# Optimization experiments

Measured on AMD Instinct MI355X. Metric: run time of the kernel, lower is better.

Reference implementation:

```python
import jax, jax.numpy as jnp
import numpy as np

N = 50000
E = 800000


def gcn_conv(x, W, b, src, dst, n_nodes):
    # PyG GCNConv: add self-loops, symmetric deg^-1/2 normalization,
    # out[dst] += norm * (x @ W)[src], then bias.
    h = x @ W  # [N, out]
    src_sl = jnp.concatenate([src, jnp.arange(n_nodes, dtype=src.dtype)])
    dst_sl = jnp.concatenate([dst, jnp.arange(n_nodes, dtype=dst.dtype)])
    deg = jax.ops.segment_sum(jnp.ones_like(dst_sl, dtype=h.dtype), dst_sl,
                              num_segments=n_nodes)  # in-degree incl. self-loop
    dinv = jnp.where(deg > 0, jax.lax.rsqrt(deg), 0.0)
    norm = dinv[src_sl] * dinv[dst_sl]  # [E+N]
    msg = norm[:, None] * h[src_sl]  # gather + scale, [E+N, out]
    out = jax.ops.segment_sum(msg, dst_sl, num_segments=n_nodes)
    return out + b


def setup_inputs() -> dict:
    key = jax.random.key(0)
    ks = jax.random.split(key, 8)
    F, H, O = 128, 128, 64
    x = jax.random.normal(ks[0], (N, F), dtype=jnp.float32)
    edge_index = jax.random.randint(ks[1], (2, E), 0, N, dtype=jnp.int64)
    # Glorot-ish scaled weights
    W1 = jax.random.normal(ks[2], (F, H), dtype=jnp.float32) / np.sqrt(F)
    b1 = jnp.zeros((H,), dtype=jnp.float32)
    W2 = jax.random.normal(ks[3], (H, H), dtype=jnp.float32) / np.sqrt(H)
    b2 = jnp.zeros((H,), dtype=jnp.float32)
    W3 = jax.random.normal(ks[4], (H, O), dtype=jnp.float32) / np.sqrt(H)
    b3 = jnp.zeros((O,), dtype=jnp.float32)
    return {"x": x, "edge_index": edge_index, "W1": W1, "b1": b1,
            "W2": W2, "b2": b2, "W3": W3, "b3": b3}


def reference(x, edge_index, W1, b1, W2, b2, W3, b3):
    src, dst = edge_index[0], edge_index[1]
    h = gcn_conv(x, W1, b1, src, dst, N)
    h = jax.nn.elu(h)
    h = gcn_conv(h, W2, b2, src, dst, N)
    h = jax.nn.elu(h)
    h = gcn_conv(h, W3, b3, src, dst, N)
    return h
```

## Files before the change

kernel.cpp:

```cpp
#include <hip/hip_runtime.h>
#include <hip/hip_fp16.h>
#include <math.h>


#define NFEAT_IN 128
#define SCAN_CHUNK 2048
#define NSHARD 8

typedef _Float16 f16x8 __attribute__((ext_vector_type(8)));
typedef float f32x4 __attribute__((ext_vector_type(4)));

__global__ void zero_kernel(int4* __restrict__ p, int n4) {
    int i = blockIdx.x * blockDim.x + threadIdx.x;
    if (i < n4) { int4 z; z.x = z.y = z.z = z.w = 0; p[i] = z; }
}

__global__ __launch_bounds__(256) void count_kernel(const int* __restrict__ dst,
                                                    int* __restrict__ cnt,
                                                    int E, int shard_sz) {
    int shard = blockIdx.x & (NSHARD - 1);
    int blk = blockIdx.x >> 3;
    int nblk = gridDim.x >> 3;
    int lo = shard * shard_sz, hi = lo + shard_sz;
    int stride = nblk * blockDim.x;
    int E4 = E >> 2;
    for (int g = blk * blockDim.x + threadIdx.x; g < E4; g += stride) {
        int4 d = *(const int4*)&dst[g * 4];
        if (d.x >= lo && d.x < hi) atomicAdd(&cnt[d.x], 1);
        if (d.y >= lo && d.y < hi) atomicAdd(&cnt[d.y], 1);
        if (d.z >= lo && d.z < hi) atomicAdd(&cnt[d.z], 1);
        if (d.w >= lo && d.w < hi) atomicAdd(&cnt[d.w], 1);
    }
    if (blockIdx.x == 0 && threadIdx.x < (E & 3)) {
        int d = dst[(E & ~3) + threadIdx.x];
        atomicAdd(&cnt[d], 1);
    }
}

__global__ __launch_bounds__(256) void reduce_kernel(const int* __restrict__ cnt,
                                                     int* __restrict__ bsum, int n) {
    __shared__ int wtot[4];
    int b = blockIdx.x, t = threadIdx.x;
    int base = b * SCAN_CHUNK + t * 8;
    int s = 0;
    if (base + 8 <= n) {
        int4 a = *(const int4*)&cnt[base];
        int4 c = *(const int4*)&cnt[base + 4];
        s = a.x + a.y + a.z + a.w + c.x + c.y + c.z + c.w;
    } else {
        for (int i = 0; i < 8; ++i) if (base + i < n) s += cnt[base + i];
    }
    int lane = t & 63, wid = t >> 6;
    #pragma unroll
    for (int off = 32; off > 0; off >>= 1) s += __shfl_down(s, off, 64);
    if (lane == 0) wtot[wid] = s;
    __syncthreads();
    if (t == 0) bsum[b] = wtot[0] + wtot[1] + wtot[2] + wtot[3];
}

__global__ void scanb_kernel(int* __restrict__ bsum, int nb, int* __restrict__ offs,
                             int n, int2* __restrict__ esw, int E) {
    int lane = threadIdx.x;
    int v = (lane < nb) ? bsum[lane] : 0;
    int inc = v;
    #pragma unroll
    for (int off = 1; off < 64; off <<= 1) {
        int t = __shfl_up(inc, off, 64);
        if (lane >= off) inc += t;
    }
    if (lane < nb) bsum[lane] = inc - v;
    if (lane == 63) offs[n] = inc;
    if (lane < 16) { int2 z; z.x = 0; z.y = 0; esw[E + lane] = z; }
}

__global__ __launch_bounds__(256) void scan3_kernel(const int* __restrict__ cnt,
                                                    const int* __restrict__ bbase,
                                                    int* __restrict__ offs,
                                                    int* __restrict__ pos,
                                                    float* __restrict__ dinv, int n) {
    __shared__ int wtot[4];
    int b = blockIdx.x, t = threadIdx.x;
    int base = b * SCAN_CHUNK + t * 8;
    int v[8];
    #pragma unroll
    for (int i = 0; i < 8; ++i) v[i] = (base + i < n) ? cnt[base + i] : 0;
    int psum[8], s = 0;
    #pragma unroll
    for (int i = 0; i < 8; ++i) { psum[i] = s; s += v[i]; }
    int lane = t & 63, wid = t >> 6;
    int inc = s;
    #pragma unroll
    for (int off = 1; off < 64; off <<= 1) {
        int tt = __shfl_up(inc, off, 64);
        if (lane >= off) inc += tt;
    }
    if (lane == 63) wtot[wid] = inc;
    __syncthreads();
    int wb = 0;
    for (int w = 0; w < wid; ++w) wb += wtot[w];
    int tbase = bbase[b] + wb + (inc - s);
    #pragma unroll
    for (int i = 0; i < 8; ++i) {
        if (base + i < n) {
            int o = tbase + psum[i];
            offs[base + i] = o;
            pos[base + i] = o;
            dinv[base + i] = rsqrtf((float)(v[i] + 1));
        }
    }
}

__global__ __launch_bounds__(256) void fill_kernel(const int* __restrict__ src,
                                                   const int* __restrict__ dst,
                                                   int* __restrict__ pos,
                                                   const float* __restrict__ dinv,
                                                   int2* __restrict__ esw,
                                                   int E, int shard_sz) {
    int shard = blockIdx.x & (NSHARD - 1);
    int blk = blockIdx.x >> 3;
    int nblk = gridDim.x >> 3;
    int lo = shard * shard_sz;
    int hi = lo + shard_sz;
    int stride = nblk * blockDim.x;
    for (int i = blk * blockDim.x + threadIdx.x; i < E; i += stride) {
        int d = dst[i];
        if (d >= lo && d < hi) {
            int s = src[i];
            int p = atomicAdd(&pos[d], 1);
            int2 e;
            e.x = s;
            e.y = __float_as_int(dinv[s]);
            esw[p] = e;
        }
    }
}

__global__ __launch_bounds__(256) void convx_kernel(const float* __restrict__ x,
                                                    f16x8* __restrict__ Xf, int nchunk) {
    int i = blockIdx.x * blockDim.x + threadIdx.x;
    if (i >= nchunk) return;
    int m = i >> 4, kc = i & 15;
    float4 a = *(const float4*)&x[(size_t)m * 128 + kc * 8];
    float4 b = *(const float4*)&x[(size_t)m * 128 + kc * 8 + 4];
    f16x8 v;
    v[0] = (_Float16)a.x; v[1] = (_Float16)a.y; v[2] = (_Float16)a.z; v[3] = (_Float16)a.w;
    v[4] = (_Float16)b.x; v[5] = (_Float16)b.y; v[6] = (_Float16)b.z; v[7] = (_Float16)b.w;
    int kt = kc >> 2, sub = kc & 3;
    Xf[(size_t)((m >> 4) * 4 + kt) * 64 + sub * 16 + (m & 15)] = v;
}

template <int NT>
__global__ void wfrag_kernel(const float* __restrict__ W, f16x8* __restrict__ Wf) {
    constexpr int BN = NT * 16;
    int c = blockIdx.x * blockDim.x + threadIdx.x;
    if (c >= NT * 4 * 64) return;
    int nt = c >> 8;
    int kt = (c >> 6) & 3;
    int l = c & 63;
    int n = nt * 16 + (l & 15);
    int k0 = kt * 32 + (l >> 4) * 8;
    f16x8 v;
    #pragma unroll
    for (int j = 0; j < 8; ++j) v[j] = (_Float16)W[(size_t)(k0 + j) * BN + n];
    Wf[c] = v;
}

template <int NT>
__global__ __launch_bounds__(256) void mgemm_kernel(const f16x8* __restrict__ Xf,
                                                    const f16x8* __restrict__ Wg,
                                                    __half* __restrict__ Y, int mtiles) {
    constexpr int BN = NT * 16;
    __shared__ f16x8 Wf[NT * 4 * 64];
    int t = threadIdx.x;
    #pragma unroll
    for (int i = 0; i < NT; ++i) Wf[t + i * 256] = Wg[t + i * 256];
    __syncthreads();
    int lane = t & 63;
    int mtile = blockIdx.x * 4 + (t >> 6);
    if (mtile >= mtiles) return;
    const f16x8* xb = Xf + (size_t)mtile * 4 * 64;
    f16x8 bf[4];
    #pragma unroll
    for (int kt = 0; kt < 4; ++kt) bf[kt] = xb[kt * 64 + lane];
    f32x4 acc[NT];
    #pragma unroll
    for (int nt = 0; nt < NT; ++nt) acc[nt] = (f32x4){0.f, 0.f, 0.f, 0.f};
    #pragma unroll
    for (int kt = 0; kt < 4; ++kt) {
        #pragma unroll
        for (int nt = 0; nt < NT; ++nt) {
            f16x8 af = Wf[(nt * 4 + kt) * 64 + lane];
            acc[nt] = __builtin_amdgcn_mfma_f32_16x16x32_f16(af, bf[kt], acc[nt], 0, 0, 0);
        }
    }
    int m = mtile * 16 + (lane & 15);
    int nc0 = (lane >> 4) * 4;
    #pragma unroll
    for (int nt = 0; nt < NT; ++nt) {
        union { __half2 h2[2]; uint2 u; } pk;
        pk.h2[0] = __floats2half2_rn(acc[nt][0], acc[nt][1]);
        pk.h2[1] = __floats2half2_rn(acc[nt][2], acc[nt][3]);
        *(uint2*)&Y[(size_t)m * BN + nt * 16 + nc0] = pk.u;
    }
}

__global__ __launch_bounds__(256) void agg128_kernel(const __half* __restrict__ H,
                                                     const int* __restrict__ offs,
                                                     const int2* __restrict__ esw,
                                                     const float* __restrict__ dinv,
                                                     const float* __restrict__ bias,
                                                     uint4* __restrict__ outf, int n) {
    int lane = threadIdx.x & 63;
    int q = lane >> 4;
    int fl = lane & 15;
    int v = blockIdx.x * 4 + (threadIdx.x >> 6);
    if (v >= n) return;
    float dv = dinv[v];
    int e0 = offs[v], e1 = offs[v + 1];
    int cntE = e1 - e0;
    int nfull = cntE >> 4;
    const char* Hb = (const char*)H + fl * 16;
    float a[8];
    #pragma unroll
    for (int k = 0; k < 8; ++k) a[k] = 0.f;
    int e = e0 + q;
    for (int i = 0; i < nfull; ++i, e += 16) {
        #pragma unroll
        for (int j = 0; j < 4; ++j) {
            int2 p = esw[e + 4 * j];
            float w = __int_as_float(p.y);
            uint4 hq = *(const uint4*)(Hb + ((size_t)(unsigned)p.x << 8));
            const _Float16* hp = (const _Float16*)&hq;
            #pragma unroll
            for (int k = 0; k < 8; ++k) a[k] = fmaf((float)hp[k], w, a[k]);
        }
    }
    if (cntE & 15) {
        #pragma unroll
        for (int j = 0; j < 4; ++j) {
            int ee = e + 4 * j;
            int2 p = esw[ee];
            float w = (ee < e1) ? __int_as_float(p.y) : 0.f;
            uint4 hq = *(const uint4*)(Hb + ((size_t)(unsigned)p.x << 8));
            const _Float16* hp = (const _Float16*)&hq;
            #pragma unroll
            for (int k = 0; k < 8; ++k) a[k] = fmaf((float)hp[k], w, a[k]);
        }
    }
    #pragma unroll
    for (int m = 16; m <= 32; m <<= 1) {
        #pragma unroll
        for (int k = 0; k < 8; ++k) a[k] += __shfl_xor(a[k], m, 64);
    }
    if (q == 0) {
        uint4 hq = *(const uint4*)(Hb + ((size_t)(unsigned)v << 8));
        const _Float16* hp = (const _Float16*)&hq;
        float b[8];
        *(float4*)&b[0] = *(const float4*)&bias[fl * 8];
        *(float4*)&b[4] = *(const float4*)&bias[fl * 8 + 4];
        float r[8];
        #pragma unroll
        for (int k = 0; k < 8; ++k) {
            float t2 = fmaf((float)hp[k], dv, a[k]);
            r[k] = fmaf(dv, t2, b[k]);
            r[k] = r[k] > 0.f ? r[k] : expm1f(r[k]);
        }
        union { __half2 h2[4]; uint4 u; } pk;
        pk.h2[0] = __floats2half2_rn(r[0], r[1]);
        pk.h2[1] = __floats2half2_rn(r[2], r[3]);
        pk.h2[2] = __floats2half2_rn(r[4], r[5]);
        pk.h2[3] = __floats2half2_rn(r[6], r[7]);
        int blockc = (v >> 4) * 4 + (fl >> 2);
        int l2 = (fl & 3) * 16 + (v & 15);
        outf[(size_t)blockc * 64 + l2] = pk.u;
    }
}

__global__ __launch_bounds__(256) void agg64_kernel(const __half* __restrict__ H,
                                                    const int* __restrict__ offs,
                                                    const int2* __restrict__ esw,
                                                    const float* __restrict__ dinv,
                                                    const float* __restrict__ bias,
                                                    float* __restrict__ out, int n) {
    int lane = threadIdx.x & 63;
    int q = lane >> 3;
    int fl = lane & 7;
    int v = blockIdx.x * 4 + (threadIdx.x >> 6);
    if (v >= n) return;
    float dv = dinv[v];
    int e0 = offs[v], e1 = offs[v + 1];
    int cntE = e1 - e0;
    int nfull = cntE >> 4;
    const char* Hb = (const char*)H + fl * 16;
    float a[8];
    #pragma unroll
    for (int k = 0; k < 8; ++k) a[k] = 0.f;
    int e = e0 + q;
    for (int i = 0; i < nfull; ++i, e += 16) {
        #pragma unroll
        for (int j = 0; j < 2; ++j) {
            int2 p = esw[e + 8 * j];
            float w = __int_as_float(p.y);
            uint4 hq = *(const uint4*)(Hb + ((size_t)(unsigned)p.x << 7));
            const _Float16* hp = (const _Float16*)&hq;
            #pragma unroll
            for (int k = 0; k < 8; ++k) a[k] = fmaf((float)hp[k], w, a[k]);
        }
    }
    if (cntE & 15) {
        #pragma unroll
        for (int j = 0; j < 2; ++j) {
            int ee = e + 8 * j;
            int2 p = esw[ee];
            float w = (ee < e1) ? __int_as_float(p.y) : 0.f;
            uint4 hq = *(const uint4*)(Hb + ((size_t)(unsigned)p.x << 7));
            const _Float16* hp = (const _Float16*)&hq;
            #pragma unroll
            for (int k = 0; k < 8; ++k) a[k] = fmaf((float)hp[k], w, a[k]);
        }
    }
    #pragma unroll
    for (int m = 8; m <= 32; m <<= 1) {
        #pragma unroll
        for (int k = 0; k < 8; ++k) a[k] += __shfl_xor(a[k], m, 64);
    }
    if (q == 0) {
        uint4 hq = *(const uint4*)(Hb + ((size_t)(unsigned)v << 7));
        const _Float16* hp = (const _Float16*)&hq;
        float b[8];
        *(float4*)&b[0] = *(const float4*)&bias[fl * 8];
        *(float4*)&b[4] = *(const float4*)&bias[fl * 8 + 4];
        float r[8];
        #pragma unroll
        for (int k = 0; k < 8; ++k) {
            float t2 = fmaf((float)hp[k], dv, a[k]);
            r[k] = fmaf(dv, t2, b[k]);
        }
        float4 o0, o1;
        o0.x = r[0]; o0.y = r[1]; o0.z = r[2]; o0.w = r[3];
        o1.x = r[4]; o1.y = r[5]; o1.z = r[6]; o1.w = r[7];
        *(float4*)&out[(size_t)v * 64 + fl * 8] = o0;
        *(float4*)&out[(size_t)v * 64 + fl * 8 + 4] = o1;
    }
}

static inline size_t alignup(size_t x) { return (x + 255) & ~(size_t)255; }

extern "C" void kernel_launch(void* const* d_in, const int* in_sizes, int n_in,
                              void* d_out, int out_size, void* d_ws, size_t ws_size,
                              hipStream_t stream) {
    const float* x  = (const float*)d_in[0];
    const int*   ei = (const int*)d_in[1];
    const float* W1 = (const float*)d_in[2];
    const float* b1 = (const float*)d_in[3];
    const float* W2 = (const float*)d_in[4];
    const float* b2 = (const float*)d_in[5];
    const float* W3 = (const float*)d_in[6];
    const float* b3 = (const float*)d_in[7];
    float* out = (float*)d_out;

    const int N = in_sizes[0] / NFEAT_IN;
    const int E = in_sizes[1] / 2;
    const int* src = ei;
    const int* dst = ei + E;

    char* w = (char*)d_ws;
    int* cnt  = (int*)w;  w += alignup((size_t)N * sizeof(int));
    int* pos  = (int*)w;  w += alignup((size_t)N * sizeof(int));
    int* offs = (int*)w;  w += alignup((size_t)(N + 1) * sizeof(int));
    float* dinv = (float*)w; w += alignup((size_t)N * sizeof(float));
    int* bsum = (int*)w;  w += alignup((size_t)64 * sizeof(int));
    int2* esw = (int2*)w; w += alignup((size_t)(E + 16) * sizeof(int2));
    __half* fA = (__half*)w; w += alignup((size_t)N * 128 * sizeof(__half));
    __half* hB = (__half*)w; w += alignup((size_t)N * 128 * sizeof(__half));
    f16x8* wf1 = (f16x8*)w; w += alignup((size_t)2048 * sizeof(f16x8));
    f16x8* wf2 = (f16x8*)w; w += alignup((size_t)2048 * sizeof(f16x8));
    f16x8* wf3 = (f16x8*)w; w += alignup((size_t)1024 * sizeof(f16x8));

    const int nb = (N + SCAN_CHUNK - 1) / SCAN_CHUNK;
    const int shard_sz = (N + NSHARD - 1) / NSHARD;
    const int mtiles = N / 16;

    zero_kernel<<<(N / 4 + 255) / 256, 256, 0, stream>>>((int4*)cnt, N / 4);
    count_kernel<<<NSHARD * 128, 256, 0, stream>>>(dst, cnt, E, shard_sz);
    reduce_kernel<<<nb, 256, 0, stream>>>(cnt, bsum, N);
    scanb_kernel<<<1, 64, 0, stream>>>(bsum, nb, offs, N, esw, E);
    scan3_kernel<<<nb, 256, 0, stream>>>(cnt, bsum, offs, pos, dinv, N);
    fill_kernel<<<NSHARD * 128, 256, 0, stream>>>(src, dst, pos, dinv, esw, E, shard_sz);

    wfrag_kernel<8><<<8, 256, 0, stream>>>(W1, wf1);
    wfrag_kernel<8><<<8, 256, 0, stream>>>(W2, wf2);
    wfrag_kernel<4><<<4, 256, 0, stream>>>(W3, wf3);
    convx_kernel<<<(N * 16 + 255) / 256, 256, 0, stream>>>(x, (f16x8*)fA, N * 16);

    int gemm_grid = (mtiles + 3) / 4;
    int agg_grid = (N + 3) / 4;

    mgemm_kernel<8><<<gemm_grid, 256, 0, stream>>>((const f16x8*)fA, wf1, hB, mtiles);
    agg128_kernel<<<agg_grid, 256, 0, stream>>>(hB, offs, esw, dinv, b1, (uint4*)fA, N);
    mgemm_kernel<8><<<gemm_grid, 256, 0, stream>>>((const f16x8*)fA, wf2, hB, mtiles);
    agg128_kernel<<<agg_grid, 256, 0, stream>>>(hB, offs, esw, dinv, b2, (uint4*)fA, N);
    mgemm_kernel<4><<<gemm_grid, 256, 0, stream>>>((const f16x8*)fA, wf3, hB, mtiles);
    agg64_kernel<<<agg_grid, 256, 0, stream>>>(hB, offs, esw, dinv, b3, out, N);
}
```

Before: 238.9 us.

## Use fp16 accumulation in aggregation, fuse scan/wfrag launches, double GEMM tiles per wave

Edge weights are now stored as a packed half2, and the 128-wide aggregation accumulates with packed half2 FMAs instead of per-element fp32 FMAs. This halves the ALU work and shuffle traffic in the main aggregation loops, at the cost of precision loss from fp16 accumulation over many edges. The single-block scanb launch is folded into scan3, where each block computes its own prefix, and the three wfrag launches become one. The ESW padding is zeroed in zero_kernel. Each GEMM wave now handles two M tiles, halving the grid and amortizing the per-block load of W into shared memory. ELU now uses __expf instead of expm1f.

After: 220.4 us. -7.7%, faster.

```diff
diff --git a/kernel.cpp b/kernel.cpp
--- a/kernel.cpp
+++ b/kernel.cpp
@@ -10,9 +10,11 @@
 typedef _Float16 f16x8 __attribute__((ext_vector_type(8)));
 typedef float f32x4 __attribute__((ext_vector_type(4)));
 
-__global__ void zero_kernel(int4* __restrict__ p, int n4) {
+__global__ void zero_kernel(int4* __restrict__ p, int n4, int4* __restrict__ eswpad) {
     int i = blockIdx.x * blockDim.x + threadIdx.x;
-    if (i < n4) { int4 z; z.x = z.y = z.z = z.w = 0; p[i] = z; }
+    int4 z; z.x = z.y = z.z = z.w = 0;
+    if (i < n4) p[i] = z;
+    if (i < 8) eswpad[i] = z;
 }
 
 __global__ __launch_bounds__(256) void count_kernel(const int* __restrict__ dst,
@@ -58,28 +60,29 @@
     if (t == 0) bsum[b] = wtot[0] + wtot[1] + wtot[2] + wtot[3];
 }
 
-__global__ void scanb_kernel(int* __restrict__ bsum, int nb, int* __restrict__ offs,
-                             int n, int2* __restrict__ esw, int E) {
-    int lane = threadIdx.x;
-    int v = (lane < nb) ? bsum[lane] : 0;
-    int inc = v;
-    #pragma unroll
-    for (int off = 1; off < 64; off <<= 1) {
-        int t = __shfl_up(inc, off, 64);
-        if (lane >= off) inc += t;
-    }
-    if (lane < nb) bsum[lane] = inc - v;
-    if (lane == 63) offs[n] = inc;
-    if (lane < 16) { int2 z; z.x = 0; z.y = 0; esw[E + lane] = z; }
-}
-
 __global__ __launch_bounds__(256) void scan3_kernel(const int* __restrict__ cnt,
-                                                    const int* __restrict__ bbase,
+                                                    const int* __restrict__ bsum,
                                                     int* __restrict__ offs,
                                                     int* __restrict__ pos,
-                                                    float* __restrict__ dinv, int n) {
+                                                    float* __restrict__ dinv,
+                                                    int n, int nb) {
     __shared__ int wtot[4];
+    __shared__ int sbase;
     int b = blockIdx.x, t = threadIdx.x;
+    if (t < 64) {
+        int val = (t < nb) ? bsum[t] : 0;
+        int pre = (t < b) ? val : 0;
+        int tot = val;
+        #pragma unroll
+        for (int off = 32; off > 0; off >>= 1) {
+            pre += __shfl_down(pre, off, 64);
+            tot += __shfl_down(tot, off, 64);
+        }
+        if (t == 0) {
+            sbase = pre;
+            if (b == nb - 1) offs[n] = tot;
+        }
+    }
     int base = b * SCAN_CHUNK + t * 8;
     int v[8];
     #pragma unroll
@@ -98,7 +101,7 @@
     __syncthreads();
     int wb = 0;
     for (int w = 0; w < wid; ++w) wb += wtot[w];
-    int tbase = bbase[b] + wb + (inc - s);
+    int tbase = sbase + wb + (inc - s);
     #pragma unroll
     for (int i = 0; i < 8; ++i) {
         if (base + i < n) {
@@ -127,9 +130,11 @@
         if (d >= lo && d < hi) {
             int s = src[i];
             int p = atomicAdd(&pos[d], 1);
+            float ds = dinv[s];
+            __half2 w2 = __floats2half2_rn(ds, ds);
             int2 e;
             e.x = s;
-            e.y = __float_as_int(dinv[s]);
+            e.y = *(int*)&w2;
             esw[p] = e;
         }
     }
@@ -149,11 +154,17 @@
     Xf[(size_t)((m >> 4) * 4 + kt) * 64 + sub * 16 + (m & 15)] = v;
 }
 
-template <int NT>
-__global__ void wfrag_kernel(const float* __restrict__ W, f16x8* __restrict__ Wf) {
-    constexpr int BN = NT * 16;
-    int c = blockIdx.x * blockDim.x + threadIdx.x;
-    if (c >= NT * 4 * 64) return;
+__global__ void wfrag_kernel(const float* __restrict__ W1, const float* __restrict__ W2,
+                             const float* __restrict__ W3, f16x8* __restrict__ wf1,
+                             f16x8* __restrict__ wf2, f16x8* __restrict__ wf3) {
+    int b = blockIdx.x;
+    const float* W; f16x8* Wf; int NT;
+    if (b < 8)       { W = W1; Wf = wf1; NT = 8; }
+    else if (b < 16) { W = W2; Wf = wf2; NT = 8; b -= 8; }
+    else             { W = W3; Wf = wf3; NT = 4; b -= 16; }
+    int c = b * 256 + threadIdx.x;
+    if (c >= NT * 256) return;
+    int BN = NT * 16;
     int nt = c >> 8;
     int kt = (c >> 6) & 3;
     int l = c & 63;
@@ -176,31 +187,35 @@
     for (int i = 0; i < NT; ++i) Wf[t + i * 256] = Wg[t + i * 256];
     __syncthreads();
     int lane = t & 63;
-    int mtile = blockIdx.x * 4 + (t >> 6);
-    if (mtile >= mtiles) return;
-    const f16x8* xb = Xf + (size_t)mtile * 4 * 64;
-    f16x8 bf[4];
-    #pragma unroll
-    for (int kt = 0; kt < 4; ++kt) bf[kt] = xb[kt * 64 + lane];
-    f32x4 acc[NT];
-    #pragma unroll
-    for (int nt = 0; nt < NT; ++nt) acc[nt] = (f32x4){0.f, 0.f, 0.f, 0.f};
-    #pragma unroll
-    for (int kt = 0; kt < 4; ++kt) {
+    int mt0 = blockIdx.x * 8 + (t >> 6) * 2;
+    #pragma unroll
+    for (int it = 0; it < 2; ++it) {
+        int mtile = mt0 + it;
+        if (mtile >= mtiles) continue;
+        const f16x8* xb = Xf + (size_t)mtile * 4 * 64;
+        f16x8 bf[4];
+        #pragma unroll
+        for (int kt = 0; kt < 4; ++kt) bf[kt] = xb[kt * 64 + lane];
+        f32x4 acc[NT];
+        #pragma unroll
+        for (int nt = 0; nt < NT; ++nt) acc[nt] = (f32x4){0.f, 0.f, 0.f, 0.f};
+        #pragma unroll
+        for (int kt = 0; kt < 4; ++kt) {
+            #pragma unroll
+            for (int nt = 0; nt < NT; ++nt) {
+                f16x8 af = Wf[(nt * 4 + kt) * 64 + lane];
+                acc[nt] = __builtin_amdgcn_mfma_f32_16x16x32_f16(af, bf[kt], acc[nt], 0, 0, 0);
+            }
+        }
+        int m = mtile * 16 + (lane & 15);
+        int nc0 = (lane >> 4) * 4;
         #pragma unroll
         for (int nt = 0; nt < NT; ++nt) {
-            f16x8 af = Wf[(nt * 4 + kt) * 64 + lane];
-            acc[nt] = __builtin_amdgcn_mfma_f32_16x16x32_f16(af, bf[kt], acc[nt], 0, 0, 0);
-        }
-    }
-    int m = mtile * 16 + (lane & 15);
-    int nc0 = (lane >> 4) * 4;
-    #pragma unroll
-    for (int nt = 0; nt < NT; ++nt) {
-        union { __half2 h2[2]; uint2 u; } pk;
-        pk.h2[0] = __floats2half2_rn(acc[nt][0], acc[nt][1]);
-        pk.h2[1] = __floats2half2_rn(acc[nt][2], acc[nt][3]);
-        *(uint2*)&Y[(size_t)m * BN + nt * 16 + nc0] = pk.u;
+            union { __half2 h2[2]; uint2 u; } pk;
+            pk.h2[0] = __floats2half2_rn(acc[nt][0], acc[nt][1]);
+            pk.h2[1] = __floats2half2_rn(acc[nt][2], acc[nt][3]);
+            *(uint2*)&Y[(size_t)m * BN + nt * 16 + nc0] = pk.u;
+        }
     }
 }
 
@@ -220,19 +235,21 @@
     int cntE = e1 - e0;
     int nfull = cntE >> 4;
     const char* Hb = (const char*)H + fl * 16;
-    float a[8];
-    #pragma unroll
-    for (int k = 0; k < 8; ++k) a[k] = 0.f;
+    __half2 acc[4];
+    __half2 zh = __floats2half2_rn(0.f, 0.f);
+    acc[0] = zh; acc[1] = zh; acc[2] = zh; acc[3] = zh;
     int e = e0 + q;
     for (int i = 0; i < nfull; ++i, e += 16) {
         #pragma unroll
         for (int j = 0; j < 4; ++j) {
             int2 p = esw[e + 4 * j];
-            float w = __int_as_float(p.y);
+            __half2 w2 = *(__half2*)&p.y;
             uint4 hq = *(const uint4*)(Hb + ((size_t)(unsigned)p.x << 8));
-            const _Float16* hp = (const _Float16*)&hq;
-            #pragma unroll
-            for (int k = 0; k < 8; ++k) a[k] = fmaf((float)hp[k], w, a[k]);
+            const __half2* h2 = (const __half2*)&hq;
+            acc[0] = __hfma2(h2[0], w2, acc[0]);
+            acc[1] = __hfma2(h2[1], w2, acc[1]);
+            acc[2] = __hfma2(h2[2], w2, acc[2]);
+            acc[3] = __hfma2(h2[3], w2, acc[3]);
         }
     }
     if (cntE & 15) {
@@ -240,19 +257,32 @@
         for (int j = 0; j < 4; ++j) {
             int ee = e + 4 * j;
             int2 p = esw[ee];
-            float w = (ee < e1) ? __int_as_float(p.y) : 0.f;
+            int wi = (ee < e1) ? p.y : 0;
+            __half2 w2 = *(__half2*)&wi;
             uint4 hq = *(const uint4*)(Hb + ((size_t)(unsigned)p.x << 8));
-            const _Float16* hp = (const _Float16*)&hq;
-            #pragma unroll
-            for (int k = 0; k < 8; ++k) a[k] = fmaf((float)hp[k], w, a[k]);
+            const __half2* h2 = (const __half2*)&hq;
+            acc[0] = __hfma2(h2[0], w2, acc[0]);
+            acc[1] = __hfma2(h2[1], w2, acc[1]);
+            acc[2] = __hfma2(h2[2], w2, acc[2]);
+            acc[3] = __hfma2(h2[3], w2, acc[3]);
         }
     }
     #pragma unroll
     for (int m = 16; m <= 32; m <<= 1) {
         #pragma unroll
-        for (int k = 0; k < 8; ++k) a[k] += __shfl_xor(a[k], m, 64);
+        for (int k = 0; k < 4; ++k) {
+            int ai = *(int*)&acc[k];
+            int bi = __shfl_xor(ai, m, 64);
+            acc[k] = __hadd2(acc[k], *(__half2*)&bi);
+        }
     }
     if (q == 0) {
+        float a[8];
+        #pragma unroll
+        for (int k = 0; k < 4; ++k) {
+            float2 f = __half22float2(acc[k]);
+            a[2 * k] = f.x; a[2 * k + 1] = f.y;
+        }
         uint4 hq = *(const uint4*)(Hb + ((size_t)(unsigned)v << 8));
         const _Float16* hp = (const _Float16*)&hq;
         float b[8];
@@ -263,7 +293,7 @@
         for (int k = 0; k < 8; ++k) {
             float t2 = fmaf((float)hp[k], dv, a[k]);
             r[k] = fmaf(dv, t2, b[k]);
-            r[k] = r[k] > 0.f ? r[k] : expm1f(r[k]);
+            r[k] = r[k] > 0.f ? r[k] : (__expf(r[k]) - 1.f);
         }
         union { __half2 h2[4]; uint4 u; } pk;
         pk.h2[0] = __floats2half2_rn(r[0], r[1]);
@@ -300,7 +330,7 @@
         #pragma unroll
         for (int j = 0; j < 2; ++j) {
             int2 p = esw[e + 8 * j];
-            float w = __int_as_float(p.y);
+            float w = __low2float(*(const __half2*)&p.y);
             uint4 hq = *(const uint4*)(Hb + ((size_t)(unsigned)p.x << 7));
             const _Float16* hp = (const _Float16*)&hq;
             #pragma unroll
@@ -312,7 +342,7 @@
         for (int j = 0; j < 2; ++j) {
             int ee = e + 8 * j;
             int2 p = esw[ee];
-            float w = (ee < e1) ? __int_as_float(p.y) : 0.f;
+            float w = (ee < e1) ? __low2float(*(const __half2*)&p.y) : 0.f;
             uint4 hq = *(const uint4*)(Hb + ((size_t)(unsigned)p.x << 7));
             const _Float16* hp = (const _Float16*)&hq;
             #pragma unroll
@@ -381,19 +411,16 @@
     const int shard_sz = (N + NSHARD - 1) / NSHARD;
     const int mtiles = N / 16;
 
-    zero_kernel<<<(N / 4 + 255) / 256, 256, 0, stream>>>((int4*)cnt, N / 4);
+    zero_kernel<<<(N / 4 + 255) / 256, 256, 0, stream>>>((int4*)cnt, N / 4, (int4*)(esw + E));
     count_kernel<<<NSHARD * 128, 256, 0, stream>>>(dst, cnt, E, shard_sz);
     reduce_kernel<<<nb, 256, 0, stream>>>(cnt, bsum, N);
-    scanb_kernel<<<1, 64, 0, stream>>>(bsum, nb, offs, N, esw, E);
-    scan3_kernel<<<nb, 256, 0, stream>>>(cnt, bsum, offs, pos, dinv, N);
+    scan3_kernel<<<nb, 256, 0, stream>>>(cnt, bsum, offs, pos, dinv, N, nb);
     fill_kernel<<<NSHARD * 128, 256, 0, stream>>>(src, dst, pos, dinv, esw, E, shard_sz);
 
-    wfrag_kernel<8><<<8, 256, 0, stream>>>(W1, wf1);
-    wfrag_kernel<8><<<8, 256, 0, stream>>>(W2, wf2);
-    wfrag_kernel<4><<<4, 256, 0, stream>>>(W3, wf3);
+    wfrag_kernel<<<20, 256, 0, stream>>>(W1, W2, W3, wf1, wf2, wf3);
     convx_kernel<<<(N * 16 + 255) / 256, 256, 0, stream>>>(x, (f16x8*)fA, N * 16);
 
-    int gemm_grid = (mtiles + 3) / 4;
+    int gemm_grid = (mtiles + 7) / 8;
     int agg_grid = (N + 3) / 4;
 
     mgemm_kernel<8><<<gemm_grid, 256, 0, stream>>>((const f16x8*)fA, wf1, hB, mtiles);
```
